# Performance work log

Measured on AMD Instinct MI355X. Metric: run time of the kernel, lower is better.

Reference implementation:

```python
import jax, jax.numpy as jnp
import numpy as np

# 5x5 Gaussian-Laplacian template: kernel = (4*GL) * GL_T, with a2=-a1/8, a3=-a1/16
GL_T = np.zeros((5, 5), np.float32)
GL_T[2, 2] = 1.0
for r, c in [(1, 2), (2, 1), (2, 3), (3, 2)]:
    GL_T[r, c] = -1.0 / 8.0
for r, c in [(0, 2), (1, 1), (1, 3), (2, 0), (2, 4), (3, 1), (3, 3), (4, 2)]:
    GL_T[r, c] = -1.0 / 16.0

SOB0 = np.array([[1, 2, 1], [0, 0, 0], [-1, -2, -1]], np.float32)
SOB45 = np.array([[2, 1, 0], [1, 0, -1], [0, -1, -2]], np.float32)
SOB90 = np.array([[1, 0, -1], [2, 0, -2], [1, 0, -1]], np.float32)
SOB135 = np.array([[0, -1, -2], [1, 0, -1], [2, 1, 0]], np.float32)

# cubic-spaced threshold value table: (10-0)*(i/100)^3, i=0..100
X_VALUES = np.array([10.0 * (i / 100.0) ** 3 for i in range(101)], np.float32)


def conv2d(x, w, stride=1, padding=0):
    return jax.lax.conv_general_dilated(
        x, w, (stride, stride), ((padding, padding), (padding, padding)),
        dimension_numbers=("NCHW", "OIHW", "NCHW"))


def avg_pool(x, k, s, p):
    # PyTorch AvgPool2d default count_include_pad=True -> divide by k*k always
    s_ = jax.lax.reduce_window(x, 0.0, jax.lax.add, (1, 1, k, k), (1, 1, s, s),
                               ((0, 0), (0, 0), (p, p), (p, p)))
    return s_ / float(k * k)


def _gdm(x, gdm_weight, conv_w, bn_gamma, bn_beta, bn_mean, bn_var):
    x = avg_pool(x, 3, 2, 1)                                  # [B,3,H/2,W/2]
    image_a = jnp.mean(x, axis=1, keepdims=True)              # [B,1,h,w]
    y = conv2d(x, conv_w, stride=2, padding=3)                # ConvBN(3,5,7,s2)
    y = (y - bn_mean[None, :, None, None]) * jax.lax.rsqrt(bn_var + 1e-5)[None, :, None, None]
    y = y * bn_gamma[None, :, None, None] + bn_beta[None, :, None, None]
    weight_att = jnp.tanh(jnp.mean(y, axis=(2, 3)))           # [B,5]

    a1 = gdm_weight[0, 0] * 4.0
    kgl = (a1 * jnp.asarray(GL_T))[None, None]                # [1,1,5,5]
    x_GL = jnp.abs(conv2d(image_a, kgl, stride=1, padding=2))
    x_GL = jnp.where(x_GL < 1e-6, 0.0, x_GL)                  # abs/threshold; relu is no-op

    b, _, h, w = x_GL.shape
    x_t = x_GL.reshape(b, 1, -1)                              # [B,1,HW]
    x_max = jnp.max(x_t, axis=-1)                             # [B,1]
    pos = x_t > 0
    all_sum = jnp.sum(pos, axis=-1)                           # [B,1]
    xv = jnp.asarray(X_VALUES)[None, :, None]                 # [1,101,1]
    sub_sum = jnp.sum(pos & (x_t <= xv), axis=-1)             # [B,101]
    percentage = sub_sum / all_sum                            # [B,101] float

    params = jnp.stack([0.2 + 0.05 * weight_att[:, 1],
                        0.4 + 0.05 * weight_att[:, 2],
                        0.6 + 0.05 * weight_att[:, 3],
                        0.8 + 0.05 * weight_att[:, 4]])       # [4,B]
    thr_pct = jnp.sort(params, axis=0).T                      # [B,4]
    z = jnp.abs(percentage[:, None, :] - thr_pct[:, :, None]) # [B,4,101]
    closest = jnp.argmin(z, axis=-1)                          # [B,4]
    threshold = jnp.asarray(X_VALUES)[closest]                # [B,4]

    tmin = jnp.concatenate([jnp.zeros_like(x_max), threshold], axis=-1)[:, :, None]  # [B,5,1]
    tmax = jnp.concatenate([threshold, x_max], axis=-1)[:, :, None]                  # [B,5,1]
    mask = ((x_t > tmin) & (x_t <= tmax)).astype(jnp.float32)                        # [B,5,HW]
    m = mask.reshape(b, 5, h, w)

    m = avg_pool(m, 9, 1, 4)
    m = avg_pool(m, 9, 1, 4)
    m = avg_pool(m, 9, 2, 4)                                  # [B,5,h/2,w/2]
    mf = m.reshape(b, 5, -1)
    mn = jnp.min(mf, axis=2, keepdims=True)
    mx = jnp.max(mf, axis=2, keepdims=True)
    return ((mf - mn) / (mx - mn)).reshape(b, 5, h // 2, w // 2)


def _hge(feat, hge_weight, fc_w, fc_b):
    # directional kernels built from entries of the learned 3x3 weight
    Sob0 = hge_weight[:, :, 0, 0][:, :, None, None]
    Sob45 = hge_weight[:, :, 0, 1][:, :, None, None]
    Sob90 = hge_weight[:, :, 0, 2][:, :, None, None]
    Sob135 = hge_weight[:, :, 1, 0][:, :, None, None]
    a1 = (hge_weight[:, :, 2, 2] * 4.0)[:, :, None, None]
    x_0 = conv2d(feat, Sob0 * jnp.asarray(SOB0), 1, 1)
    x_45 = conv2d(feat, Sob45 * jnp.asarray(SOB45), 1, 1)
    x_90 = conv2d(feat, Sob90 * jnp.asarray(SOB90), 1, 1)
    x_135 = conv2d(feat, Sob135 * jnp.asarray(SOB135), 1, 1)
    x_GL = conv2d(feat, a1 * jnp.asarray(GL_T), 1, 2)
    x_out = jnp.concatenate([x_0, x_45, x_90, x_135, x_GL], axis=1)  # [B,5*C,H,W]
    return conv2d(x_out, fc_w) + fc_b[None, :, None, None]


def setup_inputs() -> dict:
    key = jax.random.key(0)
    ks = jax.random.split(key, 6)
    return {
        "x": jax.random.normal(ks[0], (8, 3, 512, 512), jnp.float32),
        "gdm_weight": jax.random.normal(ks[1], (1, 5), jnp.float32) * 0.5,
        "conv_w": jax.random.normal(ks[2], (5, 3, 7, 7), jnp.float32) * 0.05,
        "bn_gamma": jnp.ones((5,), jnp.float32),
        "bn_beta": jnp.zeros((5,), jnp.float32),
        "bn_mean": jnp.zeros((5,), jnp.float32),
        "bn_var": jnp.ones((5,), jnp.float32),
        "feat": jax.random.normal(ks[3], (8, 64, 128, 128), jnp.float32),
        "hge_weight": jax.random.normal(ks[4], (64, 64, 3, 3), jnp.float32) * 0.05,
        "fc_w": jax.random.normal(ks[5], (64, 320, 1, 1), jnp.float32) * 0.05,
        "fc_b": jnp.zeros((64,), jnp.float32),
    }


def reference(x, gdm_weight, conv_w, bn_gamma, bn_beta, bn_mean, bn_var,
              feat, hge_weight, fc_w, fc_b):
    gdm_out = _gdm(x, gdm_weight, conv_w, bn_gamma, bn_beta, bn_mean, bn_var)
    hge_out = _hge(feat, hge_weight, fc_w, fc_b)
    return gdm_out, hge_out
```

## Files before the change

kernel.cpp:

```cpp
#include <hip/hip_runtime.h>
#include <hip/hip_bf16.h>
#include <math.h>

#define WS_AT    0
#define WS_YSUM  20480
#define WS_XMAX  20520
#define WS_HIST  20528
#define WS_MN    21376
#define WS_MX    21440
#define WS_XP    21504
#define WS_IA    1594368
#define WS_XGL   2118656

#define GDM_OUT  655360

static __device__ __forceinline__ float xv_val(int i) {
    double t = (double)i / 100.0;
    return (float)(10.0 * t * t * t);
}

__global__ __launch_bounds__(256) void k_front(const float* __restrict__ x,
                                               const float* __restrict__ hw,
                                               const float* __restrict__ fcw,
                                               float* __restrict__ xp,
                                               float* __restrict__ ia,
                                               float* __restrict__ At,
                                               float* __restrict__ zr,
                                               unsigned* __restrict__ mnb,
                                               unsigned* __restrict__ mxb) {
    int bid = blockIdx.x;
    int tid = threadIdx.x;
    if (bid < 2048) {
        int b = bid >> 8, oy = bid & 255;
        __shared__ float st[3][3][516];
#pragma unroll
        for (int q = 0; q < 9; ++q) {
            int ch = q / 3, r = q - 3 * (q / 3);
            int iy = 2 * oy - 1 + r;
            float2 v = {0.f, 0.f};
            if ((unsigned)iy < 512u)
                v = *(const float2*)&x[(((size_t)(b * 3 + ch)) << 18) + iy * 512 + 2 * tid];
            st[ch][r][1 + 2 * tid] = v.x;
            st[ch][r][2 + 2 * tid] = v.y;
        }
        if (tid < 9) { st[tid / 3][tid % 3][0] = 0.f; }
        else if (tid < 18) { int q = tid - 9; st[q / 3][q % 3][513] = 0.f; }
        __syncthreads();
        float cs[3];
#pragma unroll
        for (int ch = 0; ch < 3; ++ch) {
            float s = 0.f;
#pragma unroll
            for (int r = 0; r < 3; ++r)
#pragma unroll
                for (int k = 0; k < 3; ++k) s += st[ch][r][2 * tid + k];
            cs[ch] = s * (1.f / 9.f);
            xp[(((size_t)(b * 3 + ch)) << 16) + oy * 256 + tid] = cs[ch];
        }
        ia[(((size_t)b) << 16) + oy * 256 + tid] = (cs[0] + cs[1] + cs[2]) * (1.f / 3.f);
    } else if (bid < 2128) {
        int idx = (bid - 2048) * 256 + tid;
        int o = idx & 63; int k = idx >> 6;
        int d = k >> 6; int c = k & 63;
        const int goff[5] = {0, 1, 2, 3, 8};
        float s = 0.f;
        for (int m = 0; m < 64; ++m)
            s += fcw[o * 320 + d * 64 + m] * hw[(m * 64 + c) * 9 + goff[d]];
        At[k * 64 + o] = s * ((d == 4) ? 4.f : 1.f);
    } else {
#pragma unroll
        for (int q = 0; q < 4; ++q) {
            int i = tid + 256 * q;
            if (i < 864) zr[i] = 0.f;
        }
        if (tid < 40) mnb[tid] = 0x7f7fffffu;
        else if (tid < 80) mxb[tid - 40] = 0u;
    }
}

__global__ __launch_bounds__(512, 2) void k_mega(const float* __restrict__ xp,
                                                 const float* __restrict__ w,
                                                 float* __restrict__ ysum,
                                                 const float* __restrict__ ia,
                                                 const float* __restrict__ gdmw,
                                                 float* __restrict__ xgl,
                                                 int* __restrict__ hist,
                                                 unsigned* __restrict__ xmax,
                                                 const float* __restrict__ feat,
                                                 const float* __restrict__ At,
                                                 const float* __restrict__ fcb,
                                                 float* __restrict__ out) {
    __shared__ float wsm[735];
    __shared__ float red[512];
    __shared__ float xv[101];
    __shared__ int sh[102];
    __shared__ float ft[2][20][21];
    __shared__ float tl[2][5][256];
    __shared__ float al[2][2][5][64];
    int bid = blockIdx.x;
    int tid = threadIdx.x;
    if (bid < 512) {
        int hb = bid;
        int tile = hb & 63, b = hb >> 6;
        int ty = (tile >> 3) * 16, tx = (tile & 7) * 16;
        int grp = tid >> 8, tg = tid & 255;
        int og = tg >> 6;
        int pl = tg & 63;
        float acc[4][8];
#pragma unroll
        for (int i = 0; i < 4; ++i)
#pragma unroll
            for (int j = 0; j < 8; ++j) acc[i][j] = 0.f;

        const float* cur[3];
        int str3[3];
        bool ok[3];
#pragma unroll
        for (int j = 0; j < 3; ++j) {
            int l = tid + 512 * j;
            cur[j] = nullptr; str3[j] = 0; ok[j] = false;
            if (l < 800) {
                int ch = (l >= 400); int rem = l - ch * 400;
                int r = rem / 20, cx = rem - r * 20;
                int gy = ty - 2 + r, gx = tx - 2 + cx;
                if ((unsigned)gy < 128u && (unsigned)gx < 128u) {
                    cur[j] = feat + (((size_t)(b * 64 + ch)) << 14) + gy * 128 + gx;
                    str3[j] = 2 << 14;
                    ok[j] = true;
                }
            } else if (l < 1440) {
                int q = l - 800;
                int ch = (q >= 320); int k = q - ch * 320;
                cur[j] = At + (k >> 6) * 4096 + ch * 64 + (k & 63);
                str3[j] = 128;
                ok[j] = true;
            }
        }
        float pf[3], pf2[3];
#pragma unroll
        for (int j = 0; j < 3; ++j) {
            pf[j] = 0.f; pf2[j] = 0.f;
            if (ok[j]) { pf[j] = *cur[j]; cur[j] += str3[j];
                         pf2[j] = *cur[j]; cur[j] += str3[j]; }
        }

        for (int g = 0; g < 32; ++g) {
            int buf = g & 1;
#pragma unroll
            for (int j = 0; j < 3; ++j) {
                int l = tid + 512 * j;
                if (l < 800) {
                    int ch = (l >= 400); int rem = l - ch * 400;
                    int r = rem / 20, cx = rem - r * 20;
                    ft[ch][r][cx] = pf[j];
                } else if (l < 1440) {
                    ((float*)al[buf])[l - 800] = pf[j];
                }
            }
            __syncthreads();
#pragma unroll
            for (int j = 0; j < 3; ++j) pf[j] = pf2[j];
            if (g < 30) {
#pragma unroll
                for (int j = 0; j < 3; ++j) {
                    if (ok[j]) { pf2[j] = *cur[j]; cur[j] += str3[j]; }
                }
            }
            {
                int cy = (tg >> 4) + 2, cx = (tg & 15) + 2;
                int ch = grp;
                float fm2 = ft[ch][cy - 2][cx], f2p = ft[ch][cy + 2][cx];
                float fl2 = ft[ch][cy][cx - 2], fr2 = ft[ch][cy][cx + 2];
                float a  = ft[ch][cy - 1][cx - 1], bq = ft[ch][cy - 1][cx], cc = ft[ch][cy - 1][cx + 1];
                float dd = ft[ch][cy][cx - 1],     ee = ft[ch][cy][cx],     ffv = ft[ch][cy][cx + 1];
                float g_ = ft[ch][cy + 1][cx - 1], h  = ft[ch][cy + 1][cx], i2 = ft[ch][cy + 1][cx + 1];
                tl[ch][0][tg] = (a + 2.f * bq + cc) - (g_ + 2.f * h + i2);
                tl[ch][1][tg] = 2.f * a + bq + dd - ffv - h - 2.f * i2;
                tl[ch][2][tg] = (a - cc) + 2.f * (dd - ffv) + (g_ - i2);
                tl[ch][3][tg] = -bq - 2.f * cc + dd - ffv + 2.f * g_ + h;
                tl[ch][4][tg] = ee - 0.125f * (bq + dd + ffv + h)
                              - 0.0625f * (fm2 + a + cc + fl2 + fr2 + g_ + i2 + f2p);
            }
            __syncthreads();
#pragma unroll
            for (int ch = 0; ch < 2; ++ch) {
#pragma unroll
                for (int d = 0; d < 5; ++d) {
                    float4 a0 = *(const float4*)&al[buf][ch][d][grp * 32 + og * 8];
                    float4 a1 = *(const float4*)&al[buf][ch][d][grp * 32 + og * 8 + 4];
                    float av[8] = {a0.x, a0.y, a0.z, a0.w, a1.x, a1.y, a1.z, a1.w};
#pragma unroll
                    for (int pj = 0; pj < 4; ++pj) {
                        float tv = tl[ch][d][pl + 64 * pj];
#pragma unroll
                        for (int oi = 0; oi < 8; ++oi)
                            acc[pj][oi] = fmaf(av[oi], tv, acc[pj][oi]);
                    }
                }
            }
        }
#pragma unroll
        for (int oi = 0; oi < 8; ++oi) {
            int o = grp * 32 + og * 8 + oi;
            float bias = fcb[o];
            float* dsto = out + (((size_t)(b * 64 + o)) << 14);
#pragma unroll
            for (int pj = 0; pj < 4; ++pj) {
                int pxl = pl + 64 * pj;
                dsto[(ty + (pxl >> 4)) * 128 + tx + (pxl & 15)] = acc[pj][oi] + bias;
            }
        }
    } else if (bid < 768) {
        int cb = bid - 512;
        int b = cb >> 5;
        int p = (cb & 31) * 512 + tid;
        int oy = p >> 7, ox = p & 127;
        for (int l = tid; l < 735; l += 512) wsm[l] = w[l];
        __syncthreads();
        float s[5] = {0.f, 0.f, 0.f, 0.f, 0.f};
        for (int ic = 0; ic < 3; ++ic) {
            const float* src = xp + (((size_t)(b * 3 + ic)) << 16);
#pragma unroll
            for (int r = 0; r < 7; ++r) {
                int iy = 2 * oy - 3 + r; if ((unsigned)iy >= 256u) continue;
#pragma unroll
                for (int ss = 0; ss < 7; ++ss) {
                    int ix = 2 * ox - 3 + ss; if ((unsigned)ix >= 256u) continue;
                    float v = src[iy * 256 + ix];
                    int wi = (ic * 7 + r) * 7 + ss;
#pragma unroll
                    for (int co = 0; co < 5; ++co) s[co] = fmaf(wsm[co * 147 + wi], v, s[co]);
                }
            }
        }
#pragma unroll
        for (int co = 0; co < 5; ++co) {
            red[tid] = s[co]; __syncthreads();
            for (int off = 256; off > 0; off >>= 1) {
                if (tid < off) red[tid] += red[tid + off];
                __syncthreads();
            }
            if (tid == 0) atomicAdd(&ysum[b * 5 + co], red[0]);
            __syncthreads();
        }
    } else {
        int idx = bid - 768;
        int b = idx >> 7;
        int p = (idx & 127) * 512 + tid;
        int y = p >> 8, x = p & 255;
        if (tid < 101) xv[tid] = xv_val(tid);
        if (tid < 102) sh[tid] = 0;
        __syncthreads();
        const float* src = ia + (((size_t)b) << 16);
        float a1 = gdmw[0] * 4.f;
        auto rd = [&](int dy, int dx) -> float {
            int iy = y + dy, ix = x + dx;
            if ((unsigned)iy >= 256u || (unsigned)ix >= 256u) return 0.f;
            return src[iy * 256 + ix];
        };
        float acc = rd(0, 0)
            - 0.125f  * (rd(-1, 0) + rd(0, -1) + rd(0, 1) + rd(1, 0))
            - 0.0625f * (rd(-2, 0) + rd(-1, -1) + rd(-1, 1) + rd(0, -2) +
                         rd(0, 2) + rd(1, -1) + rd(1, 1) + rd(2, 0));
        float raw = fabsf(a1 * acc);
        float val = (raw < 1e-6f) ? 0.f : raw;
        xgl[(((size_t)b) << 16) + p] = val;
        if (val > 0.f) {
            int lo = 0, hi = 101;
            while (lo < hi) { int mid = (lo + hi) >> 1; if (val <= xv[mid]) hi = mid; else lo = mid + 1; }
            atomicAdd(&sh[lo], 1);
        }
        red[tid] = val; __syncthreads();
        for (int off = 256; off > 0; off >>= 1) {
            if (tid < off) red[tid] = fmaxf(red[tid], red[tid + off]);
            __syncthreads();
        }
        if (tid == 0) atomicMax(&xmax[b], __float_as_uint(red[0]));
        if (tid < 102 && sh[tid]) atomicAdd(&hist[b * 102 + tid], sh[tid]);
    }
}

__global__ __launch_bounds__(256) void k_pool(const float* __restrict__ xgl,
                                              const float* __restrict__ ysum,
                                              const float* __restrict__ gamma,
                                              const float* __restrict__ beta,
                                              const float* __restrict__ mean,
                                              const float* __restrict__ var,
                                              const int* __restrict__ hist,
                                              const unsigned* __restrict__ xmax,
                                              float* __restrict__ p2,
                                              unsigned* __restrict__ mnb,
                                              unsigned* __restrict__ mxb) {
    int plane = blockIdx.y;
    int r0 = blockIdx.x * 8;
    int b = plane / 5, band = plane - 5 * b;
    __shared__ float mk[39][264];
    __shared__ float p1[31][264];
    __shared__ float sthr[4];
    int tid = threadIdx.x;
    if (tid == 0) {
        float wa[5];
        for (int c = 1; c < 5; ++c) {
            float m = ysum[b * 5 + c] * (1.f / 16384.f);
            wa[c] = tanhf((m - mean[c]) * rsqrtf(var[c] + 1e-5f) * gamma[c] + beta[c]);
        }
        float pr_[4] = {0.2f + 0.05f * wa[1], 0.4f + 0.05f * wa[2],
                        0.6f + 0.05f * wa[3], 0.8f + 0.05f * wa[4]};
        auto sw = [&](int i, int j) { if (pr_[i] > pr_[j]) { float t = pr_[i]; pr_[i] = pr_[j]; pr_[j] = t; } };
        sw(0, 1); sw(2, 3); sw(0, 2); sw(1, 3); sw(1, 2);
        int all = 0;
        for (int i = 0; i <= 101; ++i) all += hist[b * 102 + i];
        float bestz[4] = {1e30f, 1e30f, 1e30f, 1e30f};
        int besti[4] = {0, 0, 0, 0};
        int cum = 0;
        for (int i = 0; i <= 100; ++i) {
            cum += hist[b * 102 + i];
            float pct = (float)cum / (float)all;
            for (int t = 0; t < 4; ++t) {
                float z = fabsf(pct - pr_[t]);
                if (z < bestz[t]) { bestz[t] = z; besti[t] = i; }
            }
        }
        for (int t = 0; t < 4; ++t) sthr[t] = xv_val(besti[t]);
    }
    __syncthreads();
    float tmin = (band == 0) ? 0.f : sthr[band - 1];
    float tmax = (band == 4) ? __uint_as_float(xmax[b]) : sthr[band];
    const float* src = xgl + (((size_t)b) << 16);
    for (int l = tid; l < 39 * 264; l += 256) {
        int i = l / 264, c = l - i * 264;
        int rr = 2 * r0 - 12 + i, cc = c - 4;
        float m = 0.f;
        if ((unsigned)rr < 256u && (unsigned)cc < 256u) {
            float v = src[rr * 256 + cc];
            m = (v > tmin && v <= tmax) ? 1.f : 0.f;
        }
        mk[i][c] = m;
    }
    __syncthreads();
    {
        int c = tid;
        auto hb = [&](int q) -> float {
            float s = 0.f;
#pragma unroll
            for (int k = 0; k < 9; ++k) s += mk[q][c + k];
            return s;
        };
        float w9[9]; float rs = 0.f;
#pragma unroll
        for (int q = 0; q < 8; ++q) { float h = hb(q); w9[q] = h; rs += h; }
#pragma unroll
        for (int pr = 0; pr < 31; ++pr) {
            int q = pr + 8;
            float h = hb(q); w9[q % 9] = h; rs += h;
            float val = rs * (1.f / 81.f);
            int ar = 2 * r0 - 8 + pr;
            if ((unsigned)ar >= 256u) val = 0.f;
            p1[pr][c + 4] = val;
            rs -= w9[pr % 9];
        }
    }
    if (tid < 248) { int i = tid >> 3, p = tid & 7; p1[i][p < 4 ? p : 256 + p] = 0.f; }
    __syncthreads();
    {
        int c = tid;
        auto hb2 = [&](int q) -> float {
            float s = 0.f;
#pragma unroll
            for (int k = 0; k < 9; ++k) s += p1[q][c + k];
            return s;
        };
        float w9[9]; float rs = 0.f;
#pragma unroll
        for (int q = 0; q < 8; ++q) { float h = hb2(q); w9[q] = h; rs += h; }
#pragma unroll
        for (int i2 = 0; i2 < 23; ++i2) {
            int q = i2 + 8;
            float h = hb2(q); w9[q % 9] = h; rs += h;
            float val = rs * (1.f / 81.f);
            int ar = 2 * r0 - 4 + i2;
            if ((unsigned)ar >= 256u) val = 0.f;
            mk[i2][c + 4] = val;
            rs -= w9[i2 % 9];
        }
    }
    if (tid < 184) { int i2 = tid >> 3, p = tid & 7; mk[i2][p < 4 ? p : 256 + p] = 0.f; }
    __syncthreads();
    for (int l = tid; l < 23 * 128; l += 256) {
        int i2 = l >> 7, ox = l & 127;
        float s = 0.f;
#pragma unroll
        for (int k = 0; k < 9; ++k) s += mk[i2][2 * ox + k];
        p1[i2][ox] = s * (1.f / 9.f);
    }
    __syncthreads();
    float vmn = 1e30f, vmx = -1e30f;
    float* dst = p2 + (size_t)plane * 16384;
#pragma unroll
    for (int q = 0; q < 4; ++q) {
        int l = tid + 256 * q;
        int jj = l >> 7, ox = l & 127;
        float s = 0.f;
#pragma unroll
        for (int k = 0; k < 9; ++k) s += p1[2 * jj + k][ox];
        s *= (1.f / 9.f);
        dst[(r0 + jj) * 128 + ox] = s;
        vmn = fminf(vmn, s); vmx = fmaxf(vmx, s);
    }
    __syncthreads();
    float* smn = &mk[0][0];
    float* smx = &mk[1][0];
    smn[tid] = vmn; smx[tid] = vmx; __syncthreads();
    for (int off = 128; off > 0; off >>= 1) {
        if (tid < off) {
            smn[tid] = fminf(smn[tid], smn[tid + off]);
            smx[tid] = fmaxf(smx[tid], smx[tid + off]);
        }
        __syncthreads();
    }
    if (tid == 0) {
        atomicMin(&mnb[plane], __float_as_uint(smn[0]));
        atomicMax(&mxb[plane], __float_as_uint(smx[0]));
    }
}

__global__ __launch_bounds__(256) void k_norm(const float* __restrict__ in,
                                              const unsigned* __restrict__ mnb,
                                              const unsigned* __restrict__ mxb,
                                              float* __restrict__ gdm) {
    int i4 = blockIdx.x * 256 + threadIdx.x;
    int idx = i4 * 4;
    int plane = idx >> 14;
    float mn = __uint_as_float(mnb[plane]), mx = __uint_as_float(mxb[plane]);
    float inv = 1.f / (mx - mn);
    float4 v = *(const float4*)&in[idx];
    float4 o = {(v.x - mn) * inv, (v.y - mn) * inv, (v.z - mn) * inv, (v.w - mn) * inv};
    *(float4*)&gdm[idx] = o;
}

extern "C" void kernel_launch(void* const* d_in, const int* in_sizes, int n_in,
                              void* d_out, int out_size, void* d_ws, size_t ws_size,
                              hipStream_t stream) {
    const float* x    = (const float*)d_in[0];
    const float* gdmw = (const float*)d_in[1];
    const float* convw= (const float*)d_in[2];
    const float* bng  = (const float*)d_in[3];
    const float* bnb  = (const float*)d_in[4];
    const float* bnm  = (const float*)d_in[5];
    const float* bnv  = (const float*)d_in[6];
    const float* feat = (const float*)d_in[7];
    const float* hw   = (const float*)d_in[8];
    const float* fcw  = (const float*)d_in[9];
    const float* fcb  = (const float*)d_in[10];
    float* out = (float*)d_out;
    float* ws  = (float*)d_ws;

    float* At   = ws + WS_AT;
    float* ysum = ws + WS_YSUM;
    unsigned* xmax = (unsigned*)(ws + WS_XMAX);
    int* hist   = (int*)(ws + WS_HIST);
    unsigned* mnb = (unsigned*)(ws + WS_MN);
    unsigned* mxb = (unsigned*)(ws + WS_MX);
    float* xp   = ws + WS_XP;
    float* ia   = ws + WS_IA;
    float* xgl  = ws + WS_XGL;
    float* p2   = ws + WS_XP + 20480;

    float* hge = out + GDM_OUT;

    k_front <<<2129, 256, 0, stream>>>(x, hw, fcw, xp, ia, At, ws + WS_YSUM, mnb, mxb);
    k_mega  <<<1792, 512, 0, stream>>>(xp, convw, ysum, ia, gdmw, xgl, hist, xmax,
                                       feat, At, fcb, hge);
    k_pool  <<<dim3(16, 40), 256, 0, stream>>>(xgl, ysum, bng, bnb, bnm, bnv, hist, xmax,
                                               p2, mnb, mxb);
    k_norm  <<<640, 256, 0, stream>>>(p2, mnb, mxb, out);
}
```

Measured before the change: 203.4 us.

## Software-pipeline HGE tile loop to one barrier per iteration with multi-buffered LDS

Restructures the HGE branch of the mega kernel so that the stencil for group g+1 and the LDS staging for group g+2 run in the same phase as the FMA accumulation for group g. The feature tile and stencil outputs are double-buffered and the weight tile is triple-buffered. This cuts the number of __syncthreads per iteration from two to one, at the cost of about twice the LDS for these arrays, which may lower occupancy.

New measurement: 244.5 us. 20.2% more time.

```diff
diff --git a/kernel.cpp b/kernel.cpp
--- a/kernel.cpp
+++ b/kernel.cpp
@@ -94,9 +94,9 @@
     __shared__ float red[512];
     __shared__ float xv[101];
     __shared__ int sh[102];
-    __shared__ float ft[2][20][21];
-    __shared__ float tl[2][5][256];
-    __shared__ float al[2][2][5][64];
+    __shared__ float ft[2][2][20][21];
+    __shared__ float tl[2][2][5][256];
+    __shared__ float al[3][2][5][64];
     int bid = blockIdx.x;
     int tid = threadIdx.x;
     if (bid < 512) {
@@ -143,61 +143,67 @@
             if (ok[j]) { pf[j] = *cur[j]; cur[j] += str3[j];
                          pf2[j] = *cur[j]; cur[j] += str3[j]; }
         }
-
-        for (int g = 0; g < 32; ++g) {
-            int buf = g & 1;
+        auto do_stage = [&](int fb, int ab) {
 #pragma unroll
             for (int j = 0; j < 3; ++j) {
                 int l = tid + 512 * j;
                 if (l < 800) {
                     int ch = (l >= 400); int rem = l - ch * 400;
                     int r = rem / 20, cx = rem - r * 20;
-                    ft[ch][r][cx] = pf[j];
+                    ft[fb][ch][r][cx] = pf[j];
                 } else if (l < 1440) {
-                    ((float*)al[buf])[l - 800] = pf[j];
+                    ((float*)al[ab])[l - 800] = pf[j];
                 }
             }
-            __syncthreads();
-#pragma unroll
-            for (int j = 0; j < 3; ++j) pf[j] = pf2[j];
-            if (g < 30) {
-#pragma unroll
-                for (int j = 0; j < 3; ++j) {
-                    if (ok[j]) { pf2[j] = *cur[j]; cur[j] += str3[j]; }
-                }
-            }
-            {
-                int cy = (tg >> 4) + 2, cx = (tg & 15) + 2;
-                int ch = grp;
-                float fm2 = ft[ch][cy - 2][cx], f2p = ft[ch][cy + 2][cx];
-                float fl2 = ft[ch][cy][cx - 2], fr2 = ft[ch][cy][cx + 2];
-                float a  = ft[ch][cy - 1][cx - 1], bq = ft[ch][cy - 1][cx], cc = ft[ch][cy - 1][cx + 1];
-                float dd = ft[ch][cy][cx - 1],     ee = ft[ch][cy][cx],     ffv = ft[ch][cy][cx + 1];
-                float g_ = ft[ch][cy + 1][cx - 1], h  = ft[ch][cy + 1][cx], i2 = ft[ch][cy + 1][cx + 1];
-                tl[ch][0][tg] = (a + 2.f * bq + cc) - (g_ + 2.f * h + i2);
-                tl[ch][1][tg] = 2.f * a + bq + dd - ffv - h - 2.f * i2;
-                tl[ch][2][tg] = (a - cc) + 2.f * (dd - ffv) + (g_ - i2);
-                tl[ch][3][tg] = -bq - 2.f * cc + dd - ffv + 2.f * g_ + h;
-                tl[ch][4][tg] = ee - 0.125f * (bq + dd + ffv + h)
+        };
+        auto rot_load = [&](bool doload) {
+#pragma unroll
+            for (int j = 0; j < 3; ++j) {
+                pf[j] = pf2[j];
+                if (doload && ok[j]) { pf2[j] = *cur[j]; cur[j] += str3[j]; }
+            }
+        };
+        auto do_stencil = [&](int sb) {
+            int cy = (tg >> 4) + 2, cx = (tg & 15) + 2;
+            int ch = grp;
+            const float (*F)[21] = ft[sb][ch];
+            float fm2 = F[cy - 2][cx], f2p = F[cy + 2][cx];
+            float fl2 = F[cy][cx - 2], fr2 = F[cy][cx + 2];
+            float a  = F[cy - 1][cx - 1], bq = F[cy - 1][cx], cc = F[cy - 1][cx + 1];
+            float dd = F[cy][cx - 1],     ee = F[cy][cx],     ffv = F[cy][cx + 1];
+            float g_ = F[cy + 1][cx - 1], h  = F[cy + 1][cx], i2 = F[cy + 1][cx + 1];
+            tl[sb][ch][0][tg] = (a + 2.f * bq + cc) - (g_ + 2.f * h + i2);
+            tl[sb][ch][1][tg] = 2.f * a + bq + dd - ffv - h - 2.f * i2;
+            tl[sb][ch][2][tg] = (a - cc) + 2.f * (dd - ffv) + (g_ - i2);
+            tl[sb][ch][3][tg] = -bq - 2.f * cc + dd - ffv + 2.f * g_ + h;
+            tl[sb][ch][4][tg] = ee - 0.125f * (bq + dd + ffv + h)
                               - 0.0625f * (fm2 + a + cc + fl2 + fr2 + g_ + i2 + f2p);
-            }
-            __syncthreads();
+        };
+        do_stage(0, 0); rot_load(true);
+        __syncthreads();
+        do_stencil(0); do_stage(1, 1); rot_load(true);
+        __syncthreads();
+        for (int g = 0; g < 32; ++g) {
+            int buf = g & 1, a3 = g % 3;
 #pragma unroll
             for (int ch = 0; ch < 2; ++ch) {
 #pragma unroll
                 for (int d = 0; d < 5; ++d) {
-                    float4 a0 = *(const float4*)&al[buf][ch][d][grp * 32 + og * 8];
-                    float4 a1 = *(const float4*)&al[buf][ch][d][grp * 32 + og * 8 + 4];
+                    float4 a0 = *(const float4*)&al[a3][ch][d][grp * 32 + og * 8];
+                    float4 a1 = *(const float4*)&al[a3][ch][d][grp * 32 + og * 8 + 4];
                     float av[8] = {a0.x, a0.y, a0.z, a0.w, a1.x, a1.y, a1.z, a1.w};
 #pragma unroll
                     for (int pj = 0; pj < 4; ++pj) {
-                        float tv = tl[ch][d][pl + 64 * pj];
+                        float tv = tl[buf][ch][d][pl + 64 * pj];
 #pragma unroll
                         for (int oi = 0; oi < 8; ++oi)
                             acc[pj][oi] = fmaf(av[oi], tv, acc[pj][oi]);
                     }
                 }
             }
+            if (g < 31) do_stencil((g + 1) & 1);
+            if (g < 30) { do_stage(buf, (g + 2) % 3); rot_load(g < 28); }
+            __syncthreads();
         }
 #pragma unroll
         for (int oi = 0; oi < 8; ++oi) {
```
